# Optimization experiments

Hardware: AMD Instinct MI355X
Metric: run time of the kernel (lower is better)

The kernel has to match this reference:

```python
import jax, jax.numpy as jnp
import numpy as np

B, T, H = 128, 2048, 256

def setup_inputs() -> dict:
    key = jax.random.key(0)
    k1, k2, k3 = jax.random.split(key, 3)
    hidden_states = jax.random.normal(k1, (B, T, H), dtype=jnp.float32)
    W_score = jax.random.normal(k2, (H, H), dtype=jnp.float32) / np.sqrt(H)
    W_att = jax.random.normal(k3, (2 * H, 128), dtype=jnp.float32) / np.sqrt(2 * H)
    return {"hidden_states": hidden_states, "W_score": W_score, "W_att": W_att}

def reference(hidden_states, W_score, W_att):
    # score_first_part: (B, T, H)
    score_first_part = jnp.einsum('bth,hk->btk', hidden_states, W_score)
    # last hidden state h_t: (B, H)
    h_t = hidden_states[:, -1, :]
    # attention scores: (B, T)
    score = jnp.einsum('bth,bh->bt', score_first_part, h_t)
    attention_weights = jax.nn.softmax(score, axis=-1)
    # context vector: (B, H)
    context_vector = jnp.einsum('bth,bt->bh', hidden_states, attention_weights)
    pre_activation = jnp.concatenate([context_vector, h_t], axis=-1)  # (B, 2H)
    attention_vector = jnp.tanh(pre_activation @ W_att)  # (B, 128)
    return attention_vector
```

## Files before the change

### kernel.cpp

```cpp
#include <hip/hip_runtime.h>
#include <math.h>

namespace {
constexpr int kB = 128;
constexpr int kT = 2048;
constexpr int kH = 256;
constexpr int kS = 16;
constexpr int kTC = kT / kS;
}

__device__ __forceinline__ float dot4(float4 a, float4 b) {
    return fmaf(a.x, b.x, fmaf(a.y, b.y, fmaf(a.z, b.z, a.w * b.w)));
}

template <int CTRL, int ROW_MASK>
__device__ __forceinline__ float dpp_add(float x) {
    int n = __builtin_amdgcn_update_dpp(0, __float_as_int(x), CTRL, ROW_MASK,
                                        0xf, true);
    return x + __int_as_float(n);
}

__device__ __forceinline__ float wave_sum(float x) {
    x = dpp_add<0xB1, 0xf>(x);
    x = dpp_add<0x4E, 0xf>(x);
    x = dpp_add<0x141, 0xf>(x);
    x = dpp_add<0x140, 0xf>(x);
    x = dpp_add<0x142, 0xa>(x);
    x = dpp_add<0x143, 0xc>(x);
    return __int_as_float(__builtin_amdgcn_readlane(__float_as_int(x), 63));
}

__global__ __launch_bounds__(256) void compute_v_kernel(
    const float* __restrict__ hs, const float* __restrict__ Wsc,
    float* __restrict__ v) {
    const int half = blockIdx.x;
    const int b = blockIdx.y;
    const int tid = threadIdx.x;
    __shared__ float sh[kH];
    sh[tid] = hs[(size_t)b * kT * kH + (size_t)(kT - 1) * kH + tid];
    __syncthreads();
    const int wv = tid >> 6, lane = tid & 63;
    const float4 hv = *reinterpret_cast<const float4*>(&sh[lane * 4]);
    #pragma unroll 4
    for (int r = 0; r < 32; ++r) {
        const int h = half * 128 + wv * 32 + r;
        const float4 wr =
            *reinterpret_cast<const float4*>(&Wsc[(size_t)h * kH + lane * 4]);
        const float s = wave_sum(dot4(wr, hv));
        if (lane == 0) v[b * kH + h] = s;
    }
}

__global__ __launch_bounds__(256) void main_pass_kernel(
    const float* __restrict__ hs, const float* __restrict__ v,
    float* __restrict__ M, float* __restrict__ L, float* __restrict__ CTX) {
    const int chunk = blockIdx.x;
    const int b = blockIdx.y;
    const int tid = threadIdx.x;
    const int wv = tid >> 6, lane = tid & 63;

    const float4 vv = *reinterpret_cast<const float4*>(&v[b * kH + lane * 4]);
    const float* base = hs + (size_t)b * kT * kH + (size_t)chunk * kTC * kH;

    float m = -INFINITY, l = 0.f;
    float4 acc = make_float4(0.f, 0.f, 0.f, 0.f);

    for (int it = 0; it < kTC / 32; ++it) {
        const float* p = base + (size_t)(it * 32 + wv * 8) * kH + lane * 4;
        float4 x[8];
        #pragma unroll
        for (int j = 0; j < 8; ++j)
            x[j] = *reinterpret_cast<const float4*>(p + j * kH);
        float s[8];
        #pragma unroll
        for (int j = 0; j < 8; ++j) s[j] = wave_sum(dot4(x[j], vv));

        float nm = m;
        #pragma unroll
        for (int j = 0; j < 8; ++j) nm = fmaxf(nm, s[j]);
        const float scale = __expf(m - nm);
        float pj[8], psum = 0.f;
        #pragma unroll
        for (int j = 0; j < 8; ++j) { pj[j] = __expf(s[j] - nm); psum += pj[j]; }
        l = fmaf(l, scale, psum);

        float ix = 0.f, iy = 0.f, iz = 0.f, iw = 0.f;
        #pragma unroll
        for (int j = 0; j < 8; ++j) {
            ix = fmaf(pj[j], x[j].x, ix);
            iy = fmaf(pj[j], x[j].y, iy);
            iz = fmaf(pj[j], x[j].z, iz);
            iw = fmaf(pj[j], x[j].w, iw);
        }
        acc.x = fmaf(acc.x, scale, ix);
        acc.y = fmaf(acc.y, scale, iy);
        acc.z = fmaf(acc.z, scale, iz);
        acc.w = fmaf(acc.w, scale, iw);
        m = nm;
    }

    __shared__ float shm[4];
    __shared__ float shl[4];
    __shared__ float shctx[4 * kH];
    if (lane == 0) { shm[wv] = m; shl[wv] = l; }
    *reinterpret_cast<float4*>(&shctx[wv * kH + lane * 4]) = acc;
    __syncthreads();

    const float m0 = shm[0], m1 = shm[1], m2 = shm[2], m3 = shm[3];
    const float gm = fmaxf(fmaxf(m0, m1), fmaxf(m2, m3));
    const float e0 = __expf(m0 - gm), e1 = __expf(m1 - gm);
    const float e2 = __expf(m2 - gm), e3 = __expf(m3 - gm);

    const int pidx = b * kS + chunk;
    const float ctx = shctx[tid] * e0 + shctx[kH + tid] * e1 +
                      shctx[2 * kH + tid] * e2 + shctx[3 * kH + tid] * e3;
    CTX[(size_t)pidx * kH + tid] = ctx;
    if (tid == 0) {
        M[pidx] = gm;
        L[pidx] = shl[0] * e0 + shl[1] * e1 + shl[2] * e2 + shl[3] * e3;
    }
}

__global__ __launch_bounds__(256) void finalize_kernel(
    const float* __restrict__ hs, const float* __restrict__ M,
    const float* __restrict__ L, const float* __restrict__ CTX,
    const float* __restrict__ Watt, float* __restrict__ out) {
    const int b = blockIdx.x;
    const int tid = threadIdx.x;
    __shared__ float pre[2 * kH];
    __shared__ float red[128];

    float gm = -INFINITY;
    #pragma unroll
    for (int c = 0; c < kS; ++c) gm = fmaxf(gm, M[b * kS + c]);
    float gl = 0.f, ctx = 0.f;
    #pragma unroll
    for (int c = 0; c < kS; ++c) {
        const float e = __expf(M[b * kS + c] - gm);
        gl = fmaf(L[b * kS + c], e, gl);
        ctx = fmaf(CTX[(size_t)(b * kS + c) * kH + tid], e, ctx);
    }
    pre[tid] = ctx / gl;
    pre[kH + tid] = hs[(size_t)b * kT * kH + (size_t)(kT - 1) * kH + tid];
    __syncthreads();

    const int j = tid & 127, half = tid >> 7;
    float s = 0.f;
    const int i0 = half * 256;
    #pragma unroll 4
    for (int i = i0; i < i0 + 256; ++i)
        s = fmaf(pre[i], Watt[(size_t)i * 128 + j], s);
    if (half == 1) red[j] = s;
    __syncthreads();
    if (half == 0) out[b * 128 + j] = tanhf(s + red[j]);
}

extern "C" void kernel_launch(void* const* d_in, const int* in_sizes, int n_in,
                              void* d_out, int out_size, void* d_ws, size_t ws_size,
                              hipStream_t stream) {
    const float* hs   = (const float*)d_in[0];
    const float* Wsc  = (const float*)d_in[1];
    const float* Watt = (const float*)d_in[2];
    float* out = (float*)d_out;

    float* ws  = (float*)d_ws;
    float* v   = ws;
    float* M   = v + kB * kH;
    float* L   = M + kB * kS;
    float* CTX = L + kB * kS;

    compute_v_kernel<<<dim3(2, kB), 256, 0, stream>>>(hs, Wsc, v);
    main_pass_kernel<<<dim3(kS, kB), 256, 0, stream>>>(hs, v, M, L, CTX);
    finalize_kernel<<<kB, 256, 0, stream>>>(hs, M, L, CTX, Watt, out);
}
```

Baseline: 399.5 us.

## Use nontemporal loads, smaller row batches, and split finalize across two blocks

The main streaming kernel now reads hidden states with nontemporal vector loads. Each wave handles 4 rows per step instead of 8, with unroll 2, and launch bounds ask for 8 blocks per CU to cut register pressure and raise occupancy. The finalize kernel is split into two blocks per batch, each covering half the output columns, with a four-way reduction over the input dimension. Together these aim to improve bandwidth use on the dominant streaming pass, at the cost of more online-softmax rescale steps per row and a finalize prologue that is now done twice.

```diff
diff --git a/kernel.cpp b/kernel.cpp
--- a/kernel.cpp
+++ b/kernel.cpp
@@ -9,8 +9,14 @@
 constexpr int kTC = kT / kS;
 }
 
-__device__ __forceinline__ float dot4(float4 a, float4 b) {
+typedef float vfloat4 __attribute__((ext_vector_type(4)));
+
+__device__ __forceinline__ float dot4v(vfloat4 a, const float4& b) {
     return fmaf(a.x, b.x, fmaf(a.y, b.y, fmaf(a.z, b.z, a.w * b.w)));
+}
+
+__device__ __forceinline__ vfloat4 nt_load4(const float* p) {
+    return __builtin_nontemporal_load(reinterpret_cast<const vfloat4*>(p));
 }
 
 template <int CTRL, int ROW_MASK>
@@ -44,14 +50,14 @@
     #pragma unroll 4
     for (int r = 0; r < 32; ++r) {
         const int h = half * 128 + wv * 32 + r;
-        const float4 wr =
-            *reinterpret_cast<const float4*>(&Wsc[(size_t)h * kH + lane * 4]);
-        const float s = wave_sum(dot4(wr, hv));
+        const vfloat4 wr =
+            *reinterpret_cast<const vfloat4*>(&Wsc[(size_t)h * kH + lane * 4]);
+        const float s = wave_sum(dot4v(wr, hv));
         if (lane == 0) v[b * kH + h] = s;
     }
 }
 
-__global__ __launch_bounds__(256) void main_pass_kernel(
+__global__ __launch_bounds__(256, 8) void main_pass_kernel(
     const float* __restrict__ hs, const float* __restrict__ v,
     float* __restrict__ M, float* __restrict__ L, float* __restrict__ CTX) {
     const int chunk = blockIdx.x;
@@ -60,43 +66,40 @@
     const int wv = tid >> 6, lane = tid & 63;
 
     const float4 vv = *reinterpret_cast<const float4*>(&v[b * kH + lane * 4]);
-    const float* base = hs + (size_t)b * kT * kH + (size_t)chunk * kTC * kH;
+    const float* p = hs + (size_t)b * kT * kH + (size_t)chunk * kTC * kH +
+                     (size_t)(wv * 4) * kH + lane * 4;
 
     float m = -INFINITY, l = 0.f;
     float4 acc = make_float4(0.f, 0.f, 0.f, 0.f);
 
-    for (int it = 0; it < kTC / 32; ++it) {
-        const float* p = base + (size_t)(it * 32 + wv * 8) * kH + lane * 4;
-        float4 x[8];
-        #pragma unroll
-        for (int j = 0; j < 8; ++j)
-            x[j] = *reinterpret_cast<const float4*>(p + j * kH);
-        float s[8];
-        #pragma unroll
-        for (int j = 0; j < 8; ++j) s[j] = wave_sum(dot4(x[j], vv));
+    #pragma unroll 2
+    for (int it = 0; it < kTC / 16; ++it) {
+        const vfloat4 x0 = nt_load4(p);
+        const vfloat4 x1 = nt_load4(p + kH);
+        const vfloat4 x2 = nt_load4(p + 2 * kH);
+        const vfloat4 x3 = nt_load4(p + 3 * kH);
+        const float s0 = wave_sum(dot4v(x0, vv));
+        const float s1 = wave_sum(dot4v(x1, vv));
+        const float s2 = wave_sum(dot4v(x2, vv));
+        const float s3 = wave_sum(dot4v(x3, vv));
 
-        float nm = m;
-        #pragma unroll
-        for (int j = 0; j < 8; ++j) nm = fmaxf(nm, s[j]);
+        const float nm = fmaxf(fmaxf(m, fmaxf(s0, s1)), fmaxf(s2, s3));
         const float scale = __expf(m - nm);
-        float pj[8], psum = 0.f;
-        #pragma unroll
-        for (int j = 0; j < 8; ++j) { pj[j] = __expf(s[j] - nm); psum += pj[j]; }
-        l = fmaf(l, scale, psum);
-
-        float ix = 0.f, iy = 0.f, iz = 0.f, iw = 0.f;
-        #pragma unroll
-        for (int j = 0; j < 8; ++j) {
-            ix = fmaf(pj[j], x[j].x, ix);
-            iy = fmaf(pj[j], x[j].y, iy);
-            iz = fmaf(pj[j], x[j].z, iz);
-            iw = fmaf(pj[j], x[j].w, iw);
-        }
-        acc.x = fmaf(acc.x, scale, ix);
-        acc.y = fmaf(acc.y, scale, iy);
-        acc.z = fmaf(acc.z, scale, iz);
-        acc.w = fmaf(acc.w, scale, iw);
+        const float p0 = __expf(s0 - nm);
+        const float p1 = __expf(s1 - nm);
+        const float p2 = __expf(s2 - nm);
+        const float p3 = __expf(s3 - nm);
+        l = fmaf(l, scale, (p0 + p1) + (p2 + p3));
+        acc.x = fmaf(acc.x, scale,
+                     fmaf(p0, x0.x, fmaf(p1, x1.x, fmaf(p2, x2.x, p3 * x3.x))));
+        acc.y = fmaf(acc.y, scale,
+                     fmaf(p0, x0.y, fmaf(p1, x1.y, fmaf(p2, x2.y, p3 * x3.y))));
+        acc.z = fmaf(acc.z, scale,
+                     fmaf(p0, x0.z, fmaf(p1, x1.z, fmaf(p2, x2.z, p3 * x3.z))));
+        acc.w = fmaf(acc.w, scale,
+                     fmaf(p0, x0.w, fmaf(p1, x1.w, fmaf(p2, x2.w, p3 * x3.w))));
         m = nm;
+        p += 16 * kH;
     }
 
     __shared__ float shm[4];
@@ -125,10 +128,11 @@
     const float* __restrict__ hs, const float* __restrict__ M,
     const float* __restrict__ L, const float* __restrict__ CTX,
     const float* __restrict__ Watt, float* __restrict__ out) {
-    const int b = blockIdx.x;
+    const int half = blockIdx.x;
+    const int b = blockIdx.y;
     const int tid = threadIdx.x;
     __shared__ float pre[2 * kH];
-    __shared__ float red[128];
+    __shared__ float red[4][64];
 
     float gm = -INFINITY;
     #pragma unroll
@@ -144,15 +148,18 @@
     pre[kH + tid] = hs[(size_t)b * kT * kH + (size_t)(kT - 1) * kH + tid];
     __syncthreads();
 
-    const int j = tid & 127, half = tid >> 7;
+    const int j = half * 64 + (tid & 63);
+    const int q = tid >> 6;
     float s = 0.f;
-    const int i0 = half * 256;
+    const int i0 = q * 128;
     #pragma unroll 4
-    for (int i = i0; i < i0 + 256; ++i)
+    for (int i = i0; i < i0 + 128; ++i)
         s = fmaf(pre[i], Watt[(size_t)i * 128 + j], s);
-    if (half == 1) red[j] = s;
+    red[q][tid & 63] = s;
     __syncthreads();
-    if (half == 0) out[b * 128 + j] = tanhf(s + red[j]);
+    if (q == 0)
+        out[b * 128 + j] =
+            tanhf((red[0][tid] + red[1][tid]) + (red[2][tid] + red[3][tid]));
 }
 
 extern "C" void kernel_launch(void* const* d_in, const int* in_sizes, int n_in,
@@ -171,5 +178,5 @@
 
     compute_v_kernel<<<dim3(2, kB), 256, 0, stream>>>(hs, Wsc, v);
     main_pass_kernel<<<dim3(kS, kB), 256, 0, stream>>>(hs, v, M, L, CTX);
-    finalize_kernel<<<kB, 256, 0, stream>>>(hs, M, L, CTX, Watt, out);
+    finalize_kernel<<<dim3(2, kB), 256, 0, stream>>>(hs, M, L, CTX, Watt, out);
 }
```

Measured after the change: 364.5 us. -8.8%, faster.
